# Kernel tuning notes

Hardware: AMD Instinct MI355X
Metric: run time of the kernel (lower is better)

Reference implementation:

```python
import jax, jax.numpy as jnp
import numpy as np

OUT_RANGE = 6.0
OUT_SHIFT = -3.0


def setup_inputs() -> dict:
    key = jax.random.key(0)
    ks = jax.random.split(key, 6)
    B, T = 128, 64
    A, V, X = 48, 48, 96
    PF = 128
    fdim = (A + 1) * (V + 1) * (X + 1)  # 232897
    return {
        "audio_h": jax.random.normal(ks[0], (B, T, A), jnp.float32),
        "video_h": jax.random.normal(ks[1], (B, T, V), jnp.float32),
        "text_h": jax.random.normal(ks[2], (B, T, X), jnp.float32),
        "W1": jax.random.normal(ks[3], (fdim, PF), jnp.float32) * 0.002,
        "b1": jnp.zeros((PF,), jnp.float32),
        "W2": jax.random.normal(ks[4], (PF, PF), jnp.float32) * 0.05,
        "b2": jnp.zeros((PF,), jnp.float32),
        "W3": jax.random.normal(ks[5], (PF, 1), jnp.float32) * 0.05,
        "b3": jnp.zeros((1,), jnp.float32),
    }


def reference(audio_h, video_h, text_h, W1, b1, W2, b2, W3, b3):
    B, T, A = audio_h.shape
    V = video_h.shape[-1]
    X = text_h.shape[-1]
    one = jnp.ones((B, T, 1), audio_h.dtype)
    a = jnp.concatenate([one, audio_h], axis=-1)  # [B,T,A+1]
    v = jnp.concatenate([one, video_h], axis=-1)  # [B,T,V+1]
    x = jnp.concatenate([one, text_h], axis=-1)   # [B,T,X+1]
    # per-timestep triple outer product, summed over t.
    # flatten order matches torch: audio slowest, then video, text fastest.
    av = jnp.einsum("bta,btv->btav", a, v).reshape(B, T, (A + 1) * (V + 1))
    fusion = jnp.einsum("btp,btx->bpx", av, x).reshape(B, -1)  # [B,(A+1)(V+1)(X+1)]
    # dropout is identity in eval mode
    h1 = jax.nn.relu(fusion @ W1 + b1)
    h2 = jax.nn.relu(h1 @ W2 + b2)
    out = jax.nn.sigmoid(h2 @ W3 + b3) * OUT_RANGE + OUT_SHIFT  # [B,1] in (-3,3)
    return out
```

## Files before the change

kernel.cpp:

```cpp
#include <hip/hip_runtime.h>


#define B_    128
#define T_    64
#define A1    49
#define V1    49
#define X1    97
#define IJ    2401
#define KTOT  232897
#define FP    232928
#define PF    128
#define KC    512
#define NB2   455

typedef short s8v __attribute__((ext_vector_type(8)));
typedef float f4v __attribute__((ext_vector_type(4)));

__device__ __forceinline__ unsigned short f2bf(float f) {
    union { float f; unsigned u; } v; v.f = f;
    return (unsigned short)((v.u + 0x7FFFu + ((v.u >> 16) & 1u)) >> 16);
}

__global__ __launch_bounds__(512) void k1_fusion(
    const float* __restrict__ audio, const float* __restrict__ video,
    const float* __restrict__ text, unsigned short* __restrict__ fusion)
{
    __shared__ float a_s[T_ * A1];
    __shared__ float v_s[T_ * V1];
    __shared__ unsigned short xT[112 * 72];
    __shared__ unsigned short w_ws[8][16 * 72];

    const int b = blockIdx.y;
    const int bx = blockIdx.x;
    const int tid = threadIdx.x;

    for (int idx = tid; idx < T_ * A1; idx += 512) {
        int t = idx / 49, i = idx - t * 49;
        a_s[idx] = (i == 0) ? 1.0f : audio[(b * T_ + t) * 48 + (i - 1)];
        v_s[idx] = (i == 0) ? 1.0f : video[(b * T_ + t) * 48 + (i - 1)];
    }
    for (int idx = tid; idx < T_ * X1; idx += 512) {
        int t = idx / 97, k = idx - t * 97;
        xT[k * 72 + t] = f2bf((k == 0) ? 1.0f : text[(b * T_ + t) * 96 + (k - 1)]);
    }
    for (int idx = tid; idx < 15 * 64; idx += 512) {
        xT[(97 + (idx >> 6)) * 72 + (idx & 63)] = 0;
    }
    __syncthreads();

    const int wave = tid >> 6, lane = tid & 63;
    const int q = lane >> 4, ln = lane & 15;
    unsigned short* w_s = w_ws[wave];

    for (int it = 0; it < 5; ++it) {
        const int tw = it * 8 + wave;
        if (tw >= 38) break;
        const int tl = bx * 38 + tw;
        if (tl >= 151) break;
        const int ij0 = tl * 16;

        #pragma unroll
        for (int ijl = 0; ijl < 16; ++ijl) {
            int ij = ij0 + ijl;
            unsigned short wv = 0;
            if (ij < IJ) {
                int i = ij / 49, j = ij - i * 49;
                wv = f2bf(a_s[lane * 49 + i] * v_s[lane * 49 + j]);
            }
            w_s[ijl * 72 + lane] = wv;
        }
        s8v af0 = *(const s8v*)&w_s[ln * 72 + q * 8];
        s8v af1 = *(const s8v*)&w_s[ln * 72 + 32 + q * 8];
        #pragma unroll
        for (int nt = 0; nt < 7; ++nt) {
            s8v bf0 = *(const s8v*)&xT[(nt * 16 + ln) * 72 + q * 8];
            s8v bf1 = *(const s8v*)&xT[(nt * 16 + ln) * 72 + 32 + q * 8];
            f4v acc = {0.f, 0.f, 0.f, 0.f};
            acc = __builtin_amdgcn_mfma_f32_16x16x32_bf16(af0, bf0, acc, 0, 0, 0);
            acc = __builtin_amdgcn_mfma_f32_16x16x32_bf16(af1, bf1, acc, 0, 0, 0);
            int kk = nt * 16 + ln;
            if (kk < X1) {
                #pragma unroll
                for (int r = 0; r < 4; ++r) {
                    int ij = ij0 + q * 4 + r;
                    if (ij < IJ)
                        fusion[(size_t)b * FP + ij * X1 + kk] = f2bf(acc[r]);
                }
            }
        }
    }
}

__global__ __launch_bounds__(256) void k2_gemm(
    const unsigned short* __restrict__ fusion, const float* __restrict__ W1,
    float* __restrict__ partials)
{
    __shared__ unsigned short A_l[128 * 40];
    __shared__ unsigned short B_l[128 * 40];

    const int blk = blockIdx.x;
    const int kbase = blk * KC;
    const int nsteps = min(KC >> 5, (FP - kbase) >> 5);
    const int tid = threadIdx.x;
    const int wave = tid >> 6, lane = tid & 63;
    const int q = lane >> 4, ln = lane & 15;

    const int mA = tid >> 1, halfA = tid & 1;
    const int fB = tid & 127, gB = tid >> 7;

    f4v acc[2][8];
    for (int h = 0; h < 2; ++h)
        for (int n = 0; n < 8; ++n) acc[h][n] = (f4v){0.f, 0.f, 0.f, 0.f};

    for (int s = 0; s < nsteps; ++s) {
        const int p0 = kbase + s * 32;
        uint4 av0 = *(const uint4*)&fusion[(size_t)mA * FP + p0 + halfA * 16];
        uint4 av1 = *(const uint4*)&fusion[(size_t)mA * FP + p0 + halfA * 16 + 8];
        float bv[16];
        #pragma unroll
        for (int c = 0; c < 16; ++c) {
            int p = p0 + gB * 16 + c;
            bv[c] = (p < KTOT) ? W1[(size_t)p * PF + fB] : 0.f;
        }
        __syncthreads();
        *(uint4*)&A_l[mA * 40 + halfA * 16] = av0;
        *(uint4*)&A_l[mA * 40 + halfA * 16 + 8] = av1;
        #pragma unroll
        for (int c = 0; c < 4; ++c) {
            ushort4 pk;
            pk.x = f2bf(bv[c * 4 + 0]); pk.y = f2bf(bv[c * 4 + 1]);
            pk.z = f2bf(bv[c * 4 + 2]); pk.w = f2bf(bv[c * 4 + 3]);
            *(ushort4*)&B_l[fB * 40 + gB * 16 + c * 4] = pk;
        }
        __syncthreads();
        s8v a0 = *(const s8v*)&A_l[(wave * 32 + ln) * 40 + q * 8];
        s8v a1 = *(const s8v*)&A_l[(wave * 32 + 16 + ln) * 40 + q * 8];
        #pragma unroll
        for (int nt = 0; nt < 8; ++nt) {
            s8v bf = *(const s8v*)&B_l[(nt * 16 + ln) * 40 + q * 8];
            acc[0][nt] = __builtin_amdgcn_mfma_f32_16x16x32_bf16(a0, bf, acc[0][nt], 0, 0, 0);
            acc[1][nt] = __builtin_amdgcn_mfma_f32_16x16x32_bf16(a1, bf, acc[1][nt], 0, 0, 0);
        }
    }

    float* outp = partials + (size_t)blk * (128 * 128);
    for (int h = 0; h < 2; ++h) {
        int mrow = wave * 32 + h * 16 + q * 4;
        for (int nt = 0; nt < 8; ++nt) {
            int f = nt * 16 + ln;
            for (int r = 0; r < 4; ++r)
                outp[(mrow + r) * 128 + f] = acc[h][nt][r];
        }
    }
}

__global__ __launch_bounds__(256) void k3_reduce(
    const float* __restrict__ partials, const float* __restrict__ b1,
    float* __restrict__ h1)
{
    __shared__ float red[256];
    const int e = blockIdx.x * 64 + (threadIdx.x & 63);
    const int rh = threadIdx.x >> 6;
    float s = 0.f;
    for (int r = rh; r < NB2; r += 4)
        s += partials[(size_t)r * 16384 + e];
    red[threadIdx.x] = s;
    __syncthreads();
    if (threadIdx.x < 64) {
        float v = red[threadIdx.x] + red[threadIdx.x + 64] +
                  red[threadIdx.x + 128] + red[threadIdx.x + 192];
        v += b1[e & 127];
        h1[e] = fmaxf(v, 0.f);
    }
}

__global__ __launch_bounds__(128) void k4_mlp(
    const float* __restrict__ h1, const float* __restrict__ W2,
    const float* __restrict__ b2, float* __restrict__ h2)
{
    __shared__ float hrow[128];
    const int b = blockIdx.x, f = threadIdx.x;
    hrow[f] = h1[b * 128 + f];
    __syncthreads();
    float s = b2[f];
    #pragma unroll 8
    for (int c = 0; c < 128; ++c) s += hrow[c] * W2[c * 128 + f];
    h2[b * 128 + f] = fmaxf(s, 0.f);
}

__global__ __launch_bounds__(128) void k5_out(
    const float* __restrict__ h2, const float* __restrict__ W3,
    const float* __restrict__ b3, float* __restrict__ out)
{
    int b = threadIdx.x;
    float s = b3[0];
    for (int c = 0; c < 128; ++c) s += h2[b * 128 + c] * W3[c];
    out[b] = 6.0f / (1.0f + expf(-s)) - 3.0f;
}

extern "C" void kernel_launch(void* const* d_in, const int* in_sizes, int n_in,
                              void* d_out, int out_size, void* d_ws, size_t ws_size,
                              hipStream_t stream)
{
    const float* audio = (const float*)d_in[0];
    const float* video = (const float*)d_in[1];
    const float* text  = (const float*)d_in[2];
    const float* W1 = (const float*)d_in[3];
    const float* b1 = (const float*)d_in[4];
    const float* W2 = (const float*)d_in[5];
    const float* b2 = (const float*)d_in[6];
    const float* W3 = (const float*)d_in[7];
    const float* b3 = (const float*)d_in[8];
    float* out = (float*)d_out;

    char* ws = (char*)d_ws;
    unsigned short* fusion = (unsigned short*)ws;
    float* partials = (float*)(ws + 59629568);
    float* h1 = (float*)(ws + 89448448);
    float* h2 = (float*)(ws + 89513984);

    k1_fusion<<<dim3(4, 128), 512, 0, stream>>>(audio, video, text, fusion);
    k2_gemm<<<dim3(NB2), 256, 0, stream>>>(fusion, W1, partials);
    k3_reduce<<<dim3(256), 256, 0, stream>>>(partials, b1, h1);
    k4_mlp<<<dim3(128), 128, 0, stream>>>(h1, W2, b2, h2);
    k5_out<<<dim3(1), 128, 0, stream>>>(h2, W3, b3, out);
}
```

Measured before the change: 277.5 us.

## Restructure split-K GEMM to load fragments directly, halve K chunk, fuse MLP tail

The W1 GEMM no longer stages data through LDS. Each of 8 waves owns 16 output features and reads its bf16 fusion fragments straight from global memory, and W1 is read with nontemporal loads. The K chunk is halved so twice as many blocks run, with a templated tail path that handles only the last block's bounds checks. The reduce kernel is retuned for the larger partial count, and the last two small MLP kernels are fused into one with a shuffle reduction. In exchange, the partials buffer doubles to about 60MB and the reduce kernel has more data to read. The fusion rows are now re-read from global by every wave instead of being shared through LDS.

```diff
diff --git a/kernel.cpp b/kernel.cpp
--- a/kernel.cpp
+++ b/kernel.cpp
@@ -10,8 +10,8 @@
 #define KTOT  232897
 #define FP    232928
 #define PF    128
-#define KC    512
-#define NB2   455
+#define KC    256
+#define NB2   910
 
 typedef short s8v __attribute__((ext_vector_type(8)));
 typedef float f4v __attribute__((ext_vector_type(4)));
@@ -91,67 +91,58 @@
     }
 }
 
-__global__ __launch_bounds__(256) void k2_gemm(
+template<bool TAIL>
+__device__ __forceinline__ void k2_body(
     const unsigned short* __restrict__ fusion, const float* __restrict__ W1,
-    float* __restrict__ partials)
-{
-    __shared__ unsigned short A_l[128 * 40];
-    __shared__ unsigned short B_l[128 * 40];
-
-    const int blk = blockIdx.x;
+    float* __restrict__ partials, int blk)
+{
     const int kbase = blk * KC;
-    const int nsteps = min(KC >> 5, (FP - kbase) >> 5);
     const int tid = threadIdx.x;
     const int wave = tid >> 6, lane = tid & 63;
     const int q = lane >> 4, ln = lane & 15;
-
-    const int mA = tid >> 1, halfA = tid & 1;
-    const int fB = tid & 127, gB = tid >> 7;
-
-    f4v acc[2][8];
-    for (int h = 0; h < 2; ++h)
-        for (int n = 0; n < 8; ++n) acc[h][n] = (f4v){0.f, 0.f, 0.f, 0.f};
-
-    for (int s = 0; s < nsteps; ++s) {
+    const int f = wave * 16 + ln;
+
+    f4v acc[8];
+    #pragma unroll
+    for (int m = 0; m < 8; ++m) acc[m] = (f4v){0.f, 0.f, 0.f, 0.f};
+
+    #pragma unroll 2
+    for (int s = 0; s < 8; ++s) {
         const int p0 = kbase + s * 32;
-        uint4 av0 = *(const uint4*)&fusion[(size_t)mA * FP + p0 + halfA * 16];
-        uint4 av1 = *(const uint4*)&fusion[(size_t)mA * FP + p0 + halfA * 16 + 8];
-        float bv[16];
-        #pragma unroll
-        for (int c = 0; c < 16; ++c) {
-            int p = p0 + gB * 16 + c;
-            bv[c] = (p < KTOT) ? W1[(size_t)p * PF + fB] : 0.f;
-        }
-        __syncthreads();
-        *(uint4*)&A_l[mA * 40 + halfA * 16] = av0;
-        *(uint4*)&A_l[mA * 40 + halfA * 16 + 8] = av1;
-        #pragma unroll
-        for (int c = 0; c < 4; ++c) {
-            ushort4 pk;
-            pk.x = f2bf(bv[c * 4 + 0]); pk.y = f2bf(bv[c * 4 + 1]);
-            pk.z = f2bf(bv[c * 4 + 2]); pk.w = f2bf(bv[c * 4 + 3]);
-            *(ushort4*)&B_l[fB * 40 + gB * 16 + c * 4] = pk;
-        }
-        __syncthreads();
-        s8v a0 = *(const s8v*)&A_l[(wave * 32 + ln) * 40 + q * 8];
-        s8v a1 = *(const s8v*)&A_l[(wave * 32 + 16 + ln) * 40 + q * 8];
-        #pragma unroll
-        for (int nt = 0; nt < 8; ++nt) {
-            s8v bf = *(const s8v*)&B_l[(nt * 16 + ln) * 40 + q * 8];
-            acc[0][nt] = __builtin_amdgcn_mfma_f32_16x16x32_bf16(a0, bf, acc[0][nt], 0, 0, 0);
-            acc[1][nt] = __builtin_amdgcn_mfma_f32_16x16x32_bf16(a1, bf, acc[1][nt], 0, 0, 0);
-        }
-    }
-
-    float* outp = partials + (size_t)blk * (128 * 128);
-    for (int h = 0; h < 2; ++h) {
-        int mrow = wave * 32 + h * 16 + q * 4;
-        for (int nt = 0; nt < 8; ++nt) {
-            int f = nt * 16 + ln;
-            for (int r = 0; r < 4; ++r)
-                outp[(mrow + r) * 128 + f] = acc[h][nt][r];
-        }
-    }
+        s8v bfrag;
+        #pragma unroll
+        for (int j = 0; j < 8; ++j) {
+            int p = p0 + q * 8 + j;
+            float w;
+            if (TAIL)
+                w = (p < KTOT) ? W1[(size_t)p * PF + f] : 0.f;
+            else
+                w = __builtin_nontemporal_load(&W1[(size_t)p * PF + f]);
+            ((unsigned short*)&bfrag)[j] = f2bf(w);
+        }
+        #pragma unroll
+        for (int m = 0; m < 8; ++m) {
+            s8v afrag = *(const s8v*)&fusion[(size_t)(m * 16 + ln) * FP + p0 + q * 8];
+            acc[m] = __builtin_amdgcn_mfma_f32_16x16x32_bf16(afrag, bfrag, acc[m], 0, 0, 0);
+        }
+    }
+
+    float* outp = partials + (size_t)blk * 16384;
+    #pragma unroll
+    for (int m = 0; m < 8; ++m) {
+        #pragma unroll
+        for (int r = 0; r < 4; ++r)
+            outp[(m * 16 + q * 4 + r) * 128 + f] = acc[m][r];
+    }
+}
+
+__global__ __launch_bounds__(512) void k2_gemm(
+    const unsigned short* __restrict__ fusion, const float* __restrict__ W1,
+    float* __restrict__ partials)
+{
+    const int blk = blockIdx.x;
+    if (blk == NB2 - 1) k2_body<true>(fusion, W1, partials, blk);
+    else                k2_body<false>(fusion, W1, partials, blk);
 }
 
 __global__ __launch_bounds__(256) void k3_reduce(
@@ -159,43 +150,48 @@
     float* __restrict__ h1)
 {
     __shared__ float red[256];
-    const int e = blockIdx.x * 64 + (threadIdx.x & 63);
-    const int rh = threadIdx.x >> 6;
-    float s = 0.f;
-    for (int r = rh; r < NB2; r += 4)
-        s += partials[(size_t)r * 16384 + e];
-    red[threadIdx.x] = s;
-    __syncthreads();
-    if (threadIdx.x < 64) {
-        float v = red[threadIdx.x] + red[threadIdx.x + 64] +
-                  red[threadIdx.x + 128] + red[threadIdx.x + 192];
+    const int e = blockIdx.x * 32 + (threadIdx.x & 31);
+    const int rh = threadIdx.x >> 5;
+    float s0 = 0.f, s1 = 0.f;
+    int r = rh;
+    for (; r + 8 < NB2; r += 16) {
+        s0 += partials[(size_t)r * 16384 + e];
+        s1 += partials[(size_t)(r + 8) * 16384 + e];
+    }
+    for (; r < NB2; r += 8) s0 += partials[(size_t)r * 16384 + e];
+    red[threadIdx.x] = s0 + s1;
+    __syncthreads();
+    if (threadIdx.x < 32) {
+        float v = 0.f;
+        #pragma unroll
+        for (int g = 0; g < 8; ++g) v += red[g * 32 + threadIdx.x];
         v += b1[e & 127];
         h1[e] = fmaxf(v, 0.f);
     }
 }
 
-__global__ __launch_bounds__(128) void k4_mlp(
+__global__ __launch_bounds__(128) void k45_tail(
     const float* __restrict__ h1, const float* __restrict__ W2,
-    const float* __restrict__ b2, float* __restrict__ h2)
+    const float* __restrict__ b2, const float* __restrict__ W3,
+    const float* __restrict__ b3, float* __restrict__ out)
 {
     __shared__ float hrow[128];
+    __shared__ float h2s[128];
     const int b = blockIdx.x, f = threadIdx.x;
     hrow[f] = h1[b * 128 + f];
     __syncthreads();
     float s = b2[f];
     #pragma unroll 8
     for (int c = 0; c < 128; ++c) s += hrow[c] * W2[c * 128 + f];
-    h2[b * 128 + f] = fmaxf(s, 0.f);
-}
-
-__global__ __launch_bounds__(128) void k5_out(
-    const float* __restrict__ h2, const float* __restrict__ W3,
-    const float* __restrict__ b3, float* __restrict__ out)
-{
-    int b = threadIdx.x;
-    float s = b3[0];
-    for (int c = 0; c < 128; ++c) s += h2[b * 128 + c] * W3[c];
-    out[b] = 6.0f / (1.0f + expf(-s)) - 3.0f;
+    h2s[f] = fmaxf(s, 0.f) * W3[f];
+    __syncthreads();
+    if (f < 64) {
+        float v = h2s[f] + h2s[f + 64];
+        #pragma unroll
+        for (int off = 32; off > 0; off >>= 1)
+            v += __shfl_down(v, off, 64);
+        if (f == 0) out[b] = 6.0f / (1.0f + expf(-(v + b3[0]))) - 3.0f;
+    }
 }
 
 extern "C" void kernel_launch(void* const* d_in, const int* in_sizes, int n_in,
@@ -216,12 +212,10 @@
     char* ws = (char*)d_ws;
     unsigned short* fusion = (unsigned short*)ws;
     float* partials = (float*)(ws + 59629568);
-    float* h1 = (float*)(ws + 89448448);
-    float* h2 = (float*)(ws + 89513984);
+    float* h1 = (float*)(ws + 119267328);
 
     k1_fusion<<<dim3(4, 128), 512, 0, stream>>>(audio, video, text, fusion);
-    k2_gemm<<<dim3(NB2), 256, 0, stream>>>(fusion, W1, partials);
-    k3_reduce<<<dim3(256), 256, 0, stream>>>(partials, b1, h1);
-    k4_mlp<<<dim3(128), 128, 0, stream>>>(h1, W2, b2, h2);
-    k5_out<<<dim3(1), 128, 0, stream>>>(h2, W3, b3, out);
-}
+    k2_gemm<<<dim3(NB2), 512, 0, stream>>>(fusion, W1, partials);
+    k3_reduce<<<dim3(512), 256, 0, stream>>>(partials, b1, h1);
+    k45_tail<<<dim3(128), 128, 0, stream>>>(h1, W2, b2, W3, b3, out);
+}
```

Result: slower. 303.8 us (+9.5%).
